# Optimization experiments

Hardware: AMD Instinct MI355X
Metric: run time of the kernel (lower is better)

Reference implementation:

```python
import jax, jax.numpy as jnp
import numpy as np

N, B, C = 2048, 2, 1024
H = 16
HD = C // H
SCALE = HD ** -0.5


def setup_inputs() -> dict:
    key = jax.random.key(0)
    k1, k2, k3 = jax.random.split(key, 3)
    x = jax.random.normal(k1, (N, B, C), dtype=jnp.float32)
    w_qkv = jax.random.normal(k2, (3 * C, C), dtype=jnp.float32) * (C ** -0.5)
    w_proj = jax.random.normal(k3, (C, C), dtype=jnp.float32) * (C ** -0.5)
    b_proj = jnp.zeros((C,), dtype=jnp.float32)
    return {"x": x, "w_qkv": w_qkv, "w_proj": w_proj, "b_proj": b_proj}


def reference(x, w_qkv, w_proj, b_proj):
    # x: (N, B, C) seq-first -> (B, N, C)
    xb = jnp.transpose(x, (1, 0, 2))
    # qkv projection (no bias), reshape to (3, B, H, N, HD)
    qkv = xb @ w_qkv.T                                  # (B, N, 3C)
    qkv = qkv.reshape(B, N, 3, H, HD).transpose(2, 0, 3, 1, 4)
    q, k, v = qkv[0], qkv[1], qkv[2]                    # each (B, H, N, HD)
    q = q * SCALE
    attn = jnp.einsum('bhnd,bhmd->bhnm', q, k)          # (B, H, N, N)
    attn = jax.nn.softmax(attn, axis=-1)
    out = jnp.einsum('bhnm,bhmd->bhnd', attn, v)        # (B, H, N, HD)
    out = out.transpose(0, 2, 1, 3).reshape(B, N, C)
    out = out @ w_proj.T + b_proj                       # (B, N, C)
    return jnp.transpose(out, (1, 0, 2))                # back to (N, B, C)
```

## Files before the change

### kernel.cpp

```cpp
#include <hip/hip_runtime.h>
#include <hip/hip_bf16.h>
#include <stdint.h>

#define N_SEQ 2048
#define BATCH 2
#define CDIM  1024
#define NH    16
#define HDIM  64
#define SM_PRESCALE 0.18033688f

typedef __attribute__((ext_vector_type(8))) short bf16x8;
typedef __attribute__((ext_vector_type(4))) float f32x4;
typedef unsigned short u16;

__device__ __forceinline__ u16 f2bf(float f) {
  union { float f; unsigned u; } v; v.f = f;
  unsigned r = v.u + 0x7fffu + ((v.u >> 16) & 1u);
  return (u16)(r >> 16);
}

__device__ __forceinline__ float exp2_fast(float x) {
  float r;
  asm("v_exp_f32 %0, %1" : "=v"(r) : "v"(x));
  return r;
}

__device__ __forceinline__ void async_copy16(void* l, const void* g) {
  __builtin_amdgcn_global_load_lds(
      (const __attribute__((address_space(1))) unsigned int*)g,
      (__attribute__((address_space(3))) unsigned int*)l, 16, 0, 0);
}

__global__ __launch_bounds__(256) void cast_f2b_kernel(
    const float* __restrict__ in, u16* __restrict__ out, int n) {
  int i = (blockIdx.x * 256 + threadIdx.x) * 4;
  if (i >= n) return;
  float4 v = *(const float4*)(in + i);
  ushort4 o;
  o.x = f2bf(v.x); o.y = f2bf(v.y); o.z = f2bf(v.z); o.w = f2bf(v.w);
  *(ushort4*)(out + i) = o;
}

__global__ __launch_bounds__(256) void cast_x_kernel(
    const float* __restrict__ x, u16* __restrict__ xb) {
  int i = blockIdx.x * 256 + threadIdx.x;
  int c  = (i & 255) << 2;
  int nb = i >> 8;
  int n = nb >> 1, b = nb & 1;
  float4 v = *(const float4*)(x + (size_t)nb * CDIM + c);
  ushort4 o;
  o.x = f2bf(v.x); o.y = f2bf(v.y); o.z = f2bf(v.z); o.w = f2bf(v.w);
  *(ushort4*)(xb + ((size_t)(b * N_SEQ + n) * CDIM) + c) = o;
}

__device__ __forceinline__ void gemm128_core(
    const u16* __restrict__ A, const u16* __restrict__ B,
    int arow0, int brow0, int K,
    u16* lA, u16* lB, f32x4 acc[4][4]) {
  const int tid = threadIdx.x;
  const int w = tid >> 6, lane = tid & 63;
  const int wm = w >> 1, wn = w & 1;
  for (int k0 = 0; k0 < K; k0 += 64) {
    __syncthreads();
    #pragma unroll
    for (int call = 0; call < 4; ++call) {
      int base = (call * 4 + w) * 64;
      int c = base + lane;
      int r = c >> 3;
      int scb = (c & 7) ^ (r & 7);
      async_copy16(lA + base * 8, A + (size_t)(arow0 + r) * K + k0 + scb * 8);
      async_copy16(lB + base * 8, B + (size_t)(brow0 + r) * K + k0 + scb * 8);
    }
    __syncthreads();
    #pragma unroll
    for (int ks = 0; ks < 2; ++ks) {
      bf16x8 af[4], bf[4];
      #pragma unroll
      for (int i = 0; i < 4; ++i) {
        int cb = ks * 4 + (lane >> 4);
        int ra = wm * 64 + i * 16 + (lane & 15);
        af[i] = *(const bf16x8*)(lA + ra * 64 + ((cb ^ (ra & 7)) << 3));
        int rb = wn * 64 + i * 16 + (lane & 15);
        bf[i] = *(const bf16x8*)(lB + rb * 64 + ((cb ^ (rb & 7)) << 3));
      }
      #pragma unroll
      for (int i = 0; i < 4; ++i)
        #pragma unroll
        for (int j = 0; j < 4; ++j)
          acc[i][j] = __builtin_amdgcn_mfma_f32_16x16x32_bf16(
              af[i], bf[j], acc[i][j], 0, 0, 0);
    }
  }
}

__global__ __launch_bounds__(256) void gemm_qkv_kernel(
    const u16* __restrict__ A, const u16* __restrict__ B,
    u16* __restrict__ qo, u16* __restrict__ ko, u16* __restrict__ vTo) {
  __shared__ __align__(16) u16 lA[128 * 64];
  __shared__ __align__(16) u16 lB[128 * 64];
  f32x4 acc[4][4] = {};
  const int arow0 = blockIdx.y * 128;
  const int brow0 = blockIdx.x * 128;
  gemm128_core(A, B, arow0, brow0, CDIM, lA, lB, acc);

  const int lane = threadIdx.x & 63;
  const int w = threadIdx.x >> 6;
  const int wm = w >> 1, wn = w & 1;
  #pragma unroll
  for (int fn = 0; fn < 4; ++fn) {
    int col0 = brow0 + wn * 64 + fn * 16;
    int sel = col0 >> 10;
    int h   = (col0 >> 6) & 15;
    int d   = (col0 & 63) + (lane & 15);
    #pragma unroll
    for (int fm = 0; fm < 4; ++fm) {
      #pragma unroll
      for (int j = 0; j < 4; ++j) {
        int row = arow0 + wm * 64 + fm * 16 + ((lane >> 4) << 2) + j;
        int b = row >> 11, n = row & (N_SEQ - 1);
        float v = acc[fm][fn][j];
        size_t head = (size_t)(b * NH + h);
        if (sel == 0)
          qo[(head * N_SEQ + n) * HDIM + d] = f2bf(v * SM_PRESCALE);
        else if (sel == 1)
          ko[(head * N_SEQ + n) * HDIM + d] = f2bf(v);
        else
          vTo[(head * HDIM + d) * N_SEQ + n] = f2bf(v);
      }
    }
  }
}

__global__ __launch_bounds__(256) void gemm_proj_kernel(
    const u16* __restrict__ A, const u16* __restrict__ B,
    const float* __restrict__ bias, float* __restrict__ out) {
  __shared__ __align__(16) u16 lA[128 * 64];
  __shared__ __align__(16) u16 lB[128 * 64];
  f32x4 acc[4][4] = {};
  const int arow0 = blockIdx.y * 128;
  const int brow0 = blockIdx.x * 128;
  gemm128_core(A, B, arow0, brow0, CDIM, lA, lB, acc);

  const int lane = threadIdx.x & 63;
  const int w = threadIdx.x >> 6;
  const int wm = w >> 1, wn = w & 1;
  #pragma unroll
  for (int fn = 0; fn < 4; ++fn) {
    int col = brow0 + wn * 64 + fn * 16 + (lane & 15);
    float bv = bias[col];
    #pragma unroll
    for (int fm = 0; fm < 4; ++fm) {
      #pragma unroll
      for (int j = 0; j < 4; ++j) {
        int row = arow0 + wm * 64 + fm * 16 + ((lane >> 4) << 2) + j;
        int b = row >> 11, n = row & (N_SEQ - 1);
        out[((size_t)n * BATCH + b) * CDIM + col] = acc[fm][fn][j] + bv;
      }
    }
  }
}

__global__ __launch_bounds__(256) void attn_kernel(
    const u16* __restrict__ q, const u16* __restrict__ k,
    const u16* __restrict__ vT, u16* __restrict__ attn_out) {
  const int tid = threadIdx.x, w = tid >> 6, lane = tid & 63;
  const int swz = (blockIdx.x & 7) * 128 + (blockIdx.x >> 3);
  const int bh = swz >> 5;
  const int qt = swz & 31;
  const int b = bh >> 4, h = bh & 15;
  const u16* Q  = q  + (size_t)bh * N_SEQ * HDIM;
  const u16* K  = k  + (size_t)bh * N_SEQ * HDIM;
  const u16* VT = vT + (size_t)bh * HDIM * N_SEQ;
  const int q0 = qt * 64;
  const int lg = lane >> 4;

  __shared__ __align__(16) u16 Ks[64 * 64];
  __shared__ __align__(16) u16 VTs[64 * 64];

  bf16x8 qa[2];
  {
    int qrow = q0 + w * 16 + (lane & 15);
    #pragma unroll
    for (int ks = 0; ks < 2; ++ks)
      qa[ks] = *(const bf16x8*)(Q + (size_t)qrow * HDIM + ks * 32 + lg * 8);
  }

  f32x4 o[4] = {};
  float m = -1e30f, l = 0.f;

  for (int kv0 = 0; kv0 < N_SEQ; kv0 += 64) {
    __syncthreads();
    #pragma unroll
    for (int call = 0; call < 2; ++call) {
      int base = (call * 4 + w) * 64;
      int c = base + lane;
      int r = c >> 3;
      int scb = (c & 7) ^ (r & 7);
      int pr = (r & 32) | ((r & 12) << 1) | ((r & 16) >> 2) | (r & 3);
      async_copy16(Ks + base * 8, K + (size_t)(kv0 + pr) * HDIM + scb * 8);
      async_copy16(VTs + base * 8, VT + (size_t)r * N_SEQ + kv0 + scb * 8);
    }
    __syncthreads();

    f32x4 s[4] = {};
    __builtin_amdgcn_s_setprio(1);
    #pragma unroll
    for (int ks = 0; ks < 2; ++ks) {
      #pragma unroll
      for (int fn = 0; fn < 4; ++fn) {
        int r = fn * 16 + (lane & 15);
        int cb = ks * 4 + lg;
        bf16x8 kb = *(const bf16x8*)(Ks + r * 64 + ((cb ^ (r & 7)) << 3));
        s[fn] = __builtin_amdgcn_mfma_f32_16x16x32_bf16(kb, qa[ks], s[fn], 0, 0, 0);
      }
    }
    __builtin_amdgcn_s_setprio(0);

    float mx = s[0][0];
    #pragma unroll
    for (int fn = 0; fn < 4; ++fn)
      #pragma unroll
      for (int j = 0; j < 4; ++j) mx = fmaxf(mx, s[fn][j]);
    mx = fmaxf(mx, __shfl_xor(mx, 16));
    mx = fmaxf(mx, __shfl_xor(mx, 32));
    if (__any(mx > m + 11.5416f)) {
      float mnew = fmaxf(m, mx);
      float corr = exp2_fast(m - mnew);
      m = mnew;
      l *= corr;
      #pragma unroll
      for (int fd = 0; fd < 4; ++fd)
        #pragma unroll
        for (int j = 0; j < 4; ++j) o[fd][j] *= corr;
    }
    float rs = 0.f;
    #pragma unroll
    for (int fn = 0; fn < 4; ++fn)
      #pragma unroll
      for (int j = 0; j < 4; ++j) {
        float p = exp2_fast(s[fn][j] - m);
        s[fn][j] = p; rs += p;
      }
    rs += __shfl_xor(rs, 16);
    rs += __shfl_xor(rs, 32);
    l += rs;

    #pragma unroll
    for (int ks = 0; ks < 2; ++ks) {
      bf16x8 pa;
      #pragma unroll
      for (int e = 0; e < 4; ++e) {
        pa[e]     = (short)f2bf(s[2 * ks][e]);
        pa[4 + e] = (short)f2bf(s[2 * ks + 1][e]);
      }
      __builtin_amdgcn_s_setprio(1);
      #pragma unroll
      for (int fd = 0; fd < 4; ++fd) {
        int rv = fd * 16 + (lane & 15);
        int cb = ks * 4 + lg;
        bf16x8 vb = *(const bf16x8*)(VTs + rv * 64 + ((cb ^ (rv & 7)) << 3));
        o[fd] = __builtin_amdgcn_mfma_f32_16x16x32_bf16(vb, pa, o[fd], 0, 0, 0);
      }
      __builtin_amdgcn_s_setprio(0);
    }
  }

  float inv = 1.0f / l;
  int qrow = q0 + w * 16 + (lane & 15);
  u16* dst = attn_out + ((size_t)(b * N_SEQ + qrow)) * CDIM + h * HDIM;
  #pragma unroll
  for (int fd = 0; fd < 4; ++fd) {
    ushort4 ov;
    ov.x = f2bf(o[fd][0] * inv);
    ov.y = f2bf(o[fd][1] * inv);
    ov.z = f2bf(o[fd][2] * inv);
    ov.w = f2bf(o[fd][3] * inv);
    *(ushort4*)(dst + fd * 16 + (lg << 2)) = ov;
  }
}

extern "C" void kernel_launch(void* const* d_in, const int* in_sizes, int n_in,
                              void* d_out, int out_size, void* d_ws, size_t ws_size,
                              hipStream_t stream) {
  (void)in_sizes; (void)n_in; (void)out_size; (void)ws_size;
  const float* x      = (const float*)d_in[0];
  const float* w_qkv  = (const float*)d_in[1];
  const float* w_proj = (const float*)d_in[2];
  const float* b_proj = (const float*)d_in[3];
  float* out = (float*)d_out;

  char* ws = (char*)d_ws;
  u16* xb     = (u16*)(ws);
  u16* wqkvb  = (u16*)(ws + 8388608);
  u16* wprojb = (u16*)(ws + 14680064);
  u16* qd     = (u16*)(ws + 16777216);
  u16* kd     = (u16*)(ws + 25165824);
  u16* vTd    = (u16*)(ws + 33554432);
  u16* attn_o = (u16*)(ws + 41943040);

  cast_f2b_kernel<<<3072, 256, 0, stream>>>(w_qkv, wqkvb, 3 * CDIM * CDIM);
  cast_f2b_kernel<<<1024, 256, 0, stream>>>(w_proj, wprojb, CDIM * CDIM);
  cast_x_kernel<<<4096, 256, 0, stream>>>(x, xb);

  gemm_qkv_kernel<<<dim3(24, 32), 256, 0, stream>>>(xb, wqkvb, qd, kd, vTd);
  attn_kernel<<<1024, 256, 0, stream>>>(qd, kd, vTd, attn_o);
  gemm_proj_kernel<<<dim3(8, 32), 256, 0, stream>>>(attn_o, wprojb, b_proj, out);
}
```

Baseline: 222.4 us.

## Double-buffer attention K/V tiles, use packed bf16 convert, shrink proj GEMM tile

The attention kernel now ping-pongs between two shared-memory K/V buffers, issuing the async load of the next tile before computing the current one, so global-memory latency overlaps with MFMA and softmax work. The scalar bf16 rounding of P and the output is replaced by the hardware v_cvt_pk_bf16_f32 packed convert. The projection GEMM is templated to a 64x128 tile, doubling its grid to 512 blocks for better CU coverage. These changes raise attention LDS use and register pressure, and the packed convert's rounding may differ slightly from the manual round-to-nearest-even.

```diff
diff --git a/kernel.cpp b/kernel.cpp
--- a/kernel.cpp
+++ b/kernel.cpp
@@ -22,6 +22,12 @@
 __device__ __forceinline__ float exp2_fast(float x) {
   float r;
   asm("v_exp_f32 %0, %1" : "=v"(r) : "v"(x));
+  return r;
+}
+
+__device__ __forceinline__ uint32_t cvtpk_bf16(float lo, float hi) {
+  uint32_t r;
+  asm("v_cvt_pk_bf16_f32 %0, %1, %2" : "=v"(r) : "v"(lo), "v"(hi));
   return r;
 }
 
@@ -53,38 +59,50 @@
   *(ushort4*)(xb + ((size_t)(b * N_SEQ + n) * CDIM) + c) = o;
 }
 
-__device__ __forceinline__ void gemm128_core(
+template<int FM>
+__device__ __forceinline__ void gemm_core_t(
     const u16* __restrict__ A, const u16* __restrict__ B,
     int arow0, int brow0, int K,
-    u16* lA, u16* lB, f32x4 acc[4][4]) {
+    u16* lA, u16* lB, f32x4 acc[FM][4]) {
   const int tid = threadIdx.x;
   const int w = tid >> 6, lane = tid & 63;
   const int wm = w >> 1, wn = w & 1;
   for (int k0 = 0; k0 < K; k0 += 64) {
     __syncthreads();
     #pragma unroll
+    for (int call = 0; call < FM; ++call) {
+      int base = (call * 4 + w) * 64;
+      int c = base + lane;
+      int r = c >> 3;
+      int scb = (c & 7) ^ (r & 7);
+      async_copy16(lA + base * 8, A + (size_t)(arow0 + r) * K + k0 + scb * 8);
+    }
+    #pragma unroll
     for (int call = 0; call < 4; ++call) {
       int base = (call * 4 + w) * 64;
       int c = base + lane;
       int r = c >> 3;
       int scb = (c & 7) ^ (r & 7);
-      async_copy16(lA + base * 8, A + (size_t)(arow0 + r) * K + k0 + scb * 8);
       async_copy16(lB + base * 8, B + (size_t)(brow0 + r) * K + k0 + scb * 8);
     }
     __syncthreads();
     #pragma unroll
     for (int ks = 0; ks < 2; ++ks) {
-      bf16x8 af[4], bf[4];
+      bf16x8 af[FM], bf[4];
+      #pragma unroll
+      for (int i = 0; i < FM; ++i) {
+        int cb = ks * 4 + (lane >> 4);
+        int ra = wm * (FM * 16) + i * 16 + (lane & 15);
+        af[i] = *(const bf16x8*)(lA + ra * 64 + ((cb ^ (ra & 7)) << 3));
+      }
       #pragma unroll
       for (int i = 0; i < 4; ++i) {
         int cb = ks * 4 + (lane >> 4);
-        int ra = wm * 64 + i * 16 + (lane & 15);
-        af[i] = *(const bf16x8*)(lA + ra * 64 + ((cb ^ (ra & 7)) << 3));
         int rb = wn * 64 + i * 16 + (lane & 15);
         bf[i] = *(const bf16x8*)(lB + rb * 64 + ((cb ^ (rb & 7)) << 3));
       }
       #pragma unroll
-      for (int i = 0; i < 4; ++i)
+      for (int i = 0; i < FM; ++i)
         #pragma unroll
         for (int j = 0; j < 4; ++j)
           acc[i][j] = __builtin_amdgcn_mfma_f32_16x16x32_bf16(
@@ -101,7 +119,7 @@
   f32x4 acc[4][4] = {};
   const int arow0 = blockIdx.y * 128;
   const int brow0 = blockIdx.x * 128;
-  gemm128_core(A, B, arow0, brow0, CDIM, lA, lB, acc);
+  gemm_core_t<4>(A, B, arow0, brow0, CDIM, lA, lB, acc);
 
   const int lane = threadIdx.x & 63;
   const int w = threadIdx.x >> 6;
@@ -134,12 +152,12 @@
 __global__ __launch_bounds__(256) void gemm_proj_kernel(
     const u16* __restrict__ A, const u16* __restrict__ B,
     const float* __restrict__ bias, float* __restrict__ out) {
-  __shared__ __align__(16) u16 lA[128 * 64];
+  __shared__ __align__(16) u16 lA[64 * 64];
   __shared__ __align__(16) u16 lB[128 * 64];
-  f32x4 acc[4][4] = {};
-  const int arow0 = blockIdx.y * 128;
+  f32x4 acc[2][4] = {};
+  const int arow0 = blockIdx.y * 64;
   const int brow0 = blockIdx.x * 128;
-  gemm128_core(A, B, arow0, brow0, CDIM, lA, lB, acc);
+  gemm_core_t<2>(A, B, arow0, brow0, CDIM, lA, lB, acc);
 
   const int lane = threadIdx.x & 63;
   const int w = threadIdx.x >> 6;
@@ -149,16 +167,93 @@
     int col = brow0 + wn * 64 + fn * 16 + (lane & 15);
     float bv = bias[col];
     #pragma unroll
-    for (int fm = 0; fm < 4; ++fm) {
+    for (int fm = 0; fm < 2; ++fm) {
       #pragma unroll
       for (int j = 0; j < 4; ++j) {
-        int row = arow0 + wm * 64 + fm * 16 + ((lane >> 4) << 2) + j;
+        int row = arow0 + wm * 32 + fm * 16 + ((lane >> 4) << 2) + j;
         int b = row >> 11, n = row & (N_SEQ - 1);
         out[((size_t)n * BATCH + b) * CDIM + col] = acc[fm][fn][j] + bv;
       }
     }
   }
 }
+
+
+#define ATTN_STAGE(KS, VS, KVOFF)                                          \
+  if ((KVOFF) < N_SEQ) {                                                   \
+    _Pragma("unroll")                                                      \
+    for (int call = 0; call < 2; ++call) {                                 \
+      int base = (call * 4 + w) * 64;                                      \
+      int c = base + lane;                                                 \
+      int r = c >> 3;                                                      \
+      int scb = (c & 7) ^ (r & 7);                                         \
+      int pr = (r & 32) | ((r & 12) << 1) | ((r & 16) >> 2) | (r & 3);     \
+      async_copy16(KS + base * 8, K + (size_t)((KVOFF) + pr) * HDIM + scb * 8); \
+      async_copy16(VS + base * 8, VT + (size_t)r * N_SEQ + (KVOFF) + scb * 8);  \
+    }                                                                      \
+  }
+
+#define ATTN_COMPUTE(KS, VS)                                               \
+  {                                                                        \
+    f32x4 s[4] = {};                                                       \
+    __builtin_amdgcn_s_setprio(1);                                         \
+    _Pragma("unroll")                                                      \
+    for (int ks = 0; ks < 2; ++ks) {                                       \
+      _Pragma("unroll")                                                    \
+      for (int fn = 0; fn < 4; ++fn) {                                     \
+        int r = fn * 16 + (lane & 15);                                     \
+        int cb = ks * 4 + lg;                                              \
+        bf16x8 kb = *(const bf16x8*)(KS + r * 64 + ((cb ^ (r & 7)) << 3)); \
+        s[fn] = __builtin_amdgcn_mfma_f32_16x16x32_bf16(kb, qa[ks], s[fn], 0, 0, 0); \
+      }                                                                    \
+    }                                                                      \
+    __builtin_amdgcn_s_setprio(0);                                         \
+    float mx = s[0][0];                                                    \
+    _Pragma("unroll")                                                      \
+    for (int fn = 0; fn < 4; ++fn)                                         \
+      _Pragma("unroll")                                                    \
+      for (int j = 0; j < 4; ++j) mx = fmaxf(mx, s[fn][j]);                \
+    mx = fmaxf(mx, __shfl_xor(mx, 16));                                    \
+    mx = fmaxf(mx, __shfl_xor(mx, 32));                                    \
+    if (__any(mx > m + 11.5416f)) {                                        \
+      float mnew = fmaxf(m, mx);                                           \
+      float corr = exp2_fast(m - mnew);                                    \
+      m = mnew;                                                            \
+      l *= corr;                                                           \
+      _Pragma("unroll")                                                    \
+      for (int fd = 0; fd < 4; ++fd)                                       \
+        _Pragma("unroll")                                                  \
+        for (int j = 0; j < 4; ++j) o[fd][j] *= corr;                      \
+    }                                                                      \
+    float rs = 0.f;                                                        \
+    _Pragma("unroll")                                                      \
+    for (int fn = 0; fn < 4; ++fn)                                         \
+      _Pragma("unroll")                                                    \
+      for (int j = 0; j < 4; ++j) {                                        \
+        float p = exp2_fast(s[fn][j] - m);                                 \
+        s[fn][j] = p; rs += p;                                             \
+      }                                                                    \
+    rs += __shfl_xor(rs, 16);                                              \
+    rs += __shfl_xor(rs, 32);                                              \
+    l += rs;                                                               \
+    _Pragma("unroll")                                                      \
+    for (int ks = 0; ks < 2; ++ks) {                                       \
+      union { bf16x8 v; uint32_t u[4]; } pa;                               \
+      pa.u[0] = cvtpk_bf16(s[2 * ks][0], s[2 * ks][1]);                    \
+      pa.u[1] = cvtpk_bf16(s[2 * ks][2], s[2 * ks][3]);                    \
+      pa.u[2] = cvtpk_bf16(s[2 * ks + 1][0], s[2 * ks + 1][1]);            \
+      pa.u[3] = cvtpk_bf16(s[2 * ks + 1][2], s[2 * ks + 1][3]);            \
+      __builtin_amdgcn_s_setprio(1);                                       \
+      _Pragma("unroll")                                                    \
+      for (int fd = 0; fd < 4; ++fd) {                                     \
+        int rv = fd * 16 + (lane & 15);                                    \
+        int cb = ks * 4 + lg;                                              \
+        bf16x8 vb = *(const bf16x8*)(VS + rv * 64 + ((cb ^ (rv & 7)) << 3)); \
+        o[fd] = __builtin_amdgcn_mfma_f32_16x16x32_bf16(vb, pa.v, o[fd], 0, 0, 0); \
+      }                                                                    \
+      __builtin_amdgcn_s_setprio(0);                                       \
+    }                                                                      \
+  }
 
 __global__ __launch_bounds__(256) void attn_kernel(
     const u16* __restrict__ q, const u16* __restrict__ k,
@@ -174,8 +269,10 @@
   const int q0 = qt * 64;
   const int lg = lane >> 4;
 
-  __shared__ __align__(16) u16 Ks[64 * 64];
-  __shared__ __align__(16) u16 VTs[64 * 64];
+  __shared__ __align__(16) u16 Ks0[64 * 64];
+  __shared__ __align__(16) u16 Ks1[64 * 64];
+  __shared__ __align__(16) u16 VTs0[64 * 64];
+  __shared__ __align__(16) u16 VTs1[64 * 64];
 
   bf16x8 qa[2];
   {
@@ -188,81 +285,15 @@
   f32x4 o[4] = {};
   float m = -1e30f, l = 0.f;
 
-  for (int kv0 = 0; kv0 < N_SEQ; kv0 += 64) {
+  ATTN_STAGE(Ks0, VTs0, 0);
+  __syncthreads();
+  for (int kv0 = 0; kv0 < N_SEQ; kv0 += 128) {
+    ATTN_STAGE(Ks1, VTs1, kv0 + 64);
+    ATTN_COMPUTE(Ks0, VTs0);
     __syncthreads();
-    #pragma unroll
-    for (int call = 0; call < 2; ++call) {
-      int base = (call * 4 + w) * 64;
-      int c = base + lane;
-      int r = c >> 3;
-      int scb = (c & 7) ^ (r & 7);
-      int pr = (r & 32) | ((r & 12) << 1) | ((r & 16) >> 2) | (r & 3);
-      async_copy16(Ks + base * 8, K + (size_t)(kv0 + pr) * HDIM + scb * 8);
-      async_copy16(VTs + base * 8, VT + (size_t)r * N_SEQ + kv0 + scb * 8);
-    }
+    ATTN_STAGE(Ks0, VTs0, kv0 + 128);
+    ATTN_COMPUTE(Ks1, VTs1);
     __syncthreads();
-
-    f32x4 s[4] = {};
-    __builtin_amdgcn_s_setprio(1);
-    #pragma unroll
-    for (int ks = 0; ks < 2; ++ks) {
-      #pragma unroll
-      for (int fn = 0; fn < 4; ++fn) {
-        int r = fn * 16 + (lane & 15);
-        int cb = ks * 4 + lg;
-        bf16x8 kb = *(const bf16x8*)(Ks + r * 64 + ((cb ^ (r & 7)) << 3));
-        s[fn] = __builtin_amdgcn_mfma_f32_16x16x32_bf16(kb, qa[ks], s[fn], 0, 0, 0);
-      }
-    }
-    __builtin_amdgcn_s_setprio(0);
-
-    float mx = s[0][0];
-    #pragma unroll
-    for (int fn = 0; fn < 4; ++fn)
-      #pragma unroll
-      for (int j = 0; j < 4; ++j) mx = fmaxf(mx, s[fn][j]);
-    mx = fmaxf(mx, __shfl_xor(mx, 16));
-    mx = fmaxf(mx, __shfl_xor(mx, 32));
-    if (__any(mx > m + 11.5416f)) {
-      float mnew = fmaxf(m, mx);
-      float corr = exp2_fast(m - mnew);
-      m = mnew;
-      l *= corr;
-      #pragma unroll
-      for (int fd = 0; fd < 4; ++fd)
-        #pragma unroll
-        for (int j = 0; j < 4; ++j) o[fd][j] *= corr;
-    }
-    float rs = 0.f;
-    #pragma unroll
-    for (int fn = 0; fn < 4; ++fn)
-      #pragma unroll
-      for (int j = 0; j < 4; ++j) {
-        float p = exp2_fast(s[fn][j] - m);
-        s[fn][j] = p; rs += p;
-      }
-    rs += __shfl_xor(rs, 16);
-    rs += __shfl_xor(rs, 32);
-    l += rs;
-
-    #pragma unroll
-    for (int ks = 0; ks < 2; ++ks) {
-      bf16x8 pa;
-      #pragma unroll
-      for (int e = 0; e < 4; ++e) {
-        pa[e]     = (short)f2bf(s[2 * ks][e]);
-        pa[4 + e] = (short)f2bf(s[2 * ks + 1][e]);
-      }
-      __builtin_amdgcn_s_setprio(1);
-      #pragma unroll
-      for (int fd = 0; fd < 4; ++fd) {
-        int rv = fd * 16 + (lane & 15);
-        int cb = ks * 4 + lg;
-        bf16x8 vb = *(const bf16x8*)(VTs + rv * 64 + ((cb ^ (rv & 7)) << 3));
-        o[fd] = __builtin_amdgcn_mfma_f32_16x16x32_bf16(vb, pa, o[fd], 0, 0, 0);
-      }
-      __builtin_amdgcn_s_setprio(0);
-    }
   }
 
   float inv = 1.0f / l;
@@ -270,12 +301,10 @@
   u16* dst = attn_out + ((size_t)(b * N_SEQ + qrow)) * CDIM + h * HDIM;
   #pragma unroll
   for (int fd = 0; fd < 4; ++fd) {
-    ushort4 ov;
-    ov.x = f2bf(o[fd][0] * inv);
-    ov.y = f2bf(o[fd][1] * inv);
-    ov.z = f2bf(o[fd][2] * inv);
-    ov.w = f2bf(o[fd][3] * inv);
-    *(ushort4*)(dst + fd * 16 + (lg << 2)) = ov;
+    uint32_t ov[2];
+    ov[0] = cvtpk_bf16(o[fd][0] * inv, o[fd][1] * inv);
+    ov[1] = cvtpk_bf16(o[fd][2] * inv, o[fd][3] * inv);
+    *(uint2*)(dst + fd * 16 + (lg << 2)) = *(uint2*)ov;
   }
 }
 
@@ -304,5 +333,5 @@
 
   gemm_qkv_kernel<<<dim3(24, 32), 256, 0, stream>>>(xb, wqkvb, qd, kd, vTd);
   attn_kernel<<<1024, 256, 0, stream>>>(qd, kd, vTd, attn_o);
-  gemm_proj_kernel<<<dim3(8, 32), 256, 0, stream>>>(attn_o, wprojb, b_proj, out);
-}
+  gemm_proj_kernel<<<dim3(8, 64), 256, 0, stream>>>(attn_o, wprojb, b_proj, out);
+}
```

Result: faster. 216.7 us (-2.5%).
